# Performance work log

Measured on AMD Instinct MI355X. Metric: run time of the kernel, lower is better.

## Reference

```python
import jax, jax.numpy as jnp
import numpy as np

N, HIDDEN, LATENT, RANK = 131072, 512, 128, 4


def setup_inputs() -> dict:
    key = jax.random.key(0)
    ks = jax.random.split(key, 7)
    s = 1.0 / np.sqrt(HIDDEN)  # fan-in scaling keeps exp(fc_d(x)) well-behaved
    return {
        "x": jax.random.normal(ks[0], (N, HIDDEN), dtype=jnp.float32),
        "W_mu": jax.random.normal(ks[1], (HIDDEN, LATENT), dtype=jnp.float32) * s,
        "b_mu": jnp.zeros((LATENT,), dtype=jnp.float32),
        "W_u": jax.random.normal(ks[2], (HIDDEN, LATENT * RANK), dtype=jnp.float32) * s,
        "b_u": jnp.zeros((LATENT * RANK,), dtype=jnp.float32),
        "W_d": jax.random.normal(ks[3], (HIDDEN, LATENT), dtype=jnp.float32) * s,
        "b_d": jnp.zeros((LATENT,), dtype=jnp.float32),
        "rank": RANK,
    }


def reference(x, W_mu, b_mu, W_u, b_u, W_d, b_d, rank):
    n, _ = x.shape
    latent_dim = W_mu.shape[1]
    # forward(): three dense projections
    mu = x @ W_mu + b_mu                                  # [N, L]
    u = (x @ W_u + b_u).reshape(n, latent_dim, rank)      # [N, L, R]
    d = jnp.exp(x @ W_d + b_d)                            # [N, L]
    # kl_divergence(): batched closed-form KL vs N(0, I), Sigma = diag(d) + U U^T
    trace_Sigma = d.sum(-1) + (u * u).sum((-2, -1))       # [N]
    mu_sq = (mu * mu).sum(-1)                             # [N]
    logdet_diag = jnp.log(d).sum(-1)                      # [N]
    M = u / jnp.sqrt(d)[..., None]                        # [N, L, R]
    MtM = jnp.einsum("nlr,nls->nrs", M, M)                # [N, R, R]
    eigvals = jnp.linalg.eigvalsh(MtM)                    # [N, R]
    logdet_Sigma = logdet_diag + jnp.log1p(eigvals).sum(-1)
    kl = 0.5 * (trace_Sigma + mu_sq - latent_dim - logdet_Sigma)
    return kl.mean()
```

## Files before the change

kernel.cpp:

```cpp
#include <hip/hip_runtime.h>
#include <stdint.h>

typedef __attribute__((ext_vector_type(8))) short bf16x8;
typedef __attribute__((ext_vector_type(4))) float f32x4;

#define NROWS 131072
#define HID   512
#define LAT   128
#define NCOL  768
#define BM    64

static __device__ __forceinline__ short f2bf(float f) {
    union { float f; uint32_t u; } v; v.f = f;
    uint32_t r = v.u + 0x7FFFu + ((v.u >> 16) & 1u);
    return (short)(r >> 16);
}

__global__ void prep_kernel(const float* __restrict__ Wmu, const float* __restrict__ bmu,
                            const float* __restrict__ Wu,  const float* __restrict__ bu,
                            const float* __restrict__ Wd,  const float* __restrict__ bd,
                            short* __restrict__ Bfrag, float* __restrict__ bias,
                            float* __restrict__ out) {
    int t = blockIdx.x * blockDim.x + threadIdx.x;
    const int NFRAG = 48 * 16 * 64;
    if (t < NFRAG) {
        int l  = t & 63;
        int ks = (t >> 6) & 15;
        int n  = t >> 10;
        int col = n * 16 + (l & 15);
        int k0  = ks * 32 + (l >> 4) * 8;
        const float* src; int sc, ld;
        if (col < LAT)          { src = Wmu; sc = col;           ld = LAT;     }
        else if (col < LAT * 5) { src = Wu;  sc = col - LAT;     ld = LAT * 4; }
        else                    { src = Wd;  sc = col - LAT * 5; ld = LAT;     }
        bf16x8 v;
        #pragma unroll
        for (int j = 0; j < 8; ++j) v[j] = f2bf(src[(size_t)(k0 + j) * ld + sc]);
        ((bf16x8*)Bfrag)[t] = v;
    } else if (t < NFRAG + NCOL) {
        int col = t - NFRAG;
        float b;
        if (col < LAT)          b = bmu[col];
        else if (col < LAT * 5) b = bu[col - LAT];
        else                    b = bd[col - LAT * 5];
        bias[col] = b;
    } else if (t == NFRAG + NCOL) {
        *out = 0.0f;
    }
}

__launch_bounds__(512, 2)
__global__ void fused_kernel(const float* __restrict__ x, const short* __restrict__ Bfrag,
                             const float* __restrict__ bias, float* __restrict__ out) {
    __shared__ __align__(16) short Abuf[2][4096];
    __shared__ __align__(16) float Epi[32 * 772];
    __shared__ float bsum;

    const int tid  = threadIdx.x;
    const int l    = tid & 63;
    const int w    = tid >> 6;
    const int row0 = blockIdx.x * BM;

    const int srt  = w & 3;
    const int sks  = w >> 2;
    const int srow = srt * 16 + (l & 15);
    const int skk  = sks * 32 + (l >> 4) * 8;
    const int awr  = ((sks * 4 + srt) * 64 + l) * 8;

    const float*  xrow = x + (size_t)(row0 + srow) * HID + skk;
    const bf16x8* bwp  = (const bf16x8*)Bfrag + (size_t)w * 6 * 16 * 64 + l;

    f32x4 acc[4][6];
    #pragma unroll
    for (int rt = 0; rt < 4; ++rt)
        #pragma unroll
        for (int i = 0; i < 6; ++i) acc[rt][i] = (f32x4){0.f, 0.f, 0.f, 0.f};

    bf16x8 b0[6], b1[6];
    #pragma unroll
    for (int i = 0; i < 6; ++i) b0[i] = bwp[(size_t)i * 16 * 64];

    {
        f32x4 q0 = *(const f32x4*)(xrow);
        f32x4 q1 = *(const f32x4*)(xrow + 4);
        bf16x8 av;
        av[0]=f2bf(q0[0]); av[1]=f2bf(q0[1]); av[2]=f2bf(q0[2]); av[3]=f2bf(q0[3]);
        av[4]=f2bf(q1[0]); av[5]=f2bf(q1[1]); av[6]=f2bf(q1[2]); av[7]=f2bf(q1[3]);
        *(bf16x8*)&Abuf[0][awr] = av;
    }
    if (tid == 0) bsum = 0.0f;
    __syncthreads();

    f32x4 p0, p1;
    #pragma unroll
    for (int c = 0; c < 8; ++c) {
        const int buf = c & 1;
        #pragma unroll
        for (int i = 0; i < 6; ++i) b1[i] = bwp[((size_t)i * 16 + (2 * c + 1)) * 64];
        if (c < 7) {
            const float* xq = xrow + (c + 1) * 64;
            p0 = *(const f32x4*)(xq);
            p1 = *(const f32x4*)(xq + 4);
        }
        #pragma unroll
        for (int rt = 0; rt < 4; ++rt) {
            bf16x8 av = *(const bf16x8*)&Abuf[buf][(rt * 64 + l) * 8];
            #pragma unroll
            for (int i = 0; i < 6; ++i)
                acc[rt][i] = __builtin_amdgcn_mfma_f32_16x16x32_bf16(av, b0[i], acc[rt][i], 0, 0, 0);
        }
        if (c < 7) {
            #pragma unroll
            for (int i = 0; i < 6; ++i) b0[i] = bwp[((size_t)i * 16 + (2 * c + 2)) * 64];
        }
        #pragma unroll
        for (int rt = 0; rt < 4; ++rt) {
            bf16x8 av = *(const bf16x8*)&Abuf[buf][((4 + rt) * 64 + l) * 8];
            #pragma unroll
            for (int i = 0; i < 6; ++i)
                acc[rt][i] = __builtin_amdgcn_mfma_f32_16x16x32_bf16(av, b1[i], acc[rt][i], 0, 0, 0);
        }
        if (c < 7) {
            bf16x8 av;
            av[0]=f2bf(p0[0]); av[1]=f2bf(p0[1]); av[2]=f2bf(p0[2]); av[3]=f2bf(p0[3]);
            av[4]=f2bf(p1[0]); av[5]=f2bf(p1[1]); av[6]=f2bf(p1[2]); av[7]=f2bf(p1[3]);
            *(bf16x8*)&Abuf[buf ^ 1][awr] = av;
            __syncthreads();
        }
    }

    float pre_bias[6];
    #pragma unroll
    for (int i = 0; i < 6; ++i) pre_bias[i] = bias[(w * 6 + i) * 16 + (l & 15)];

    float my_kl = 0.0f;
    const int r16 = tid >> 4;
    const int jj  = tid & 15;

    #pragma unroll
    for (int pass = 0; pass < 2; ++pass) {
        #pragma unroll
        for (int rt2 = 0; rt2 < 2; ++rt2) {
            const int rt    = pass * 2 + rt2;
            const int rbase = rt2 * 16 + (l >> 4) * 4;
            #pragma unroll
            for (int i = 0; i < 6; ++i) {
                const int col = (w * 6 + i) * 16 + (l & 15);
                #pragma unroll
                for (int j = 0; j < 4; ++j)
                    Epi[(rbase + j) * 772 + col] = acc[rt][i][j] + pre_bias[i];
            }
        }
        __syncthreads();

        const float* rowp = &Epi[r16 * 772];
        float s_mu2=0.f, s_u2=0.f, s_d=0.f, s_td=0.f;
        float m00=0.f,m01=0.f,m02=0.f,m03=0.f,m11=0.f,m12=0.f,m13=0.f,m22=0.f,m23=0.f,m33=0.f;
        #pragma unroll
        for (int t8 = 0; t8 < 8; ++t8) {
            const int a = jj + 16 * t8;
            float mu = rowp[a];
            float td = rowp[640 + a];
            f32x4 u4 = *(const f32x4*)&rowp[128 + 4 * a];
            s_mu2 += mu * mu;
            s_td  += td;
            float ed  = __expf(td);
            float eid = __expf(-td);
            s_d  += ed;
            s_u2 += u4[0]*u4[0] + u4[1]*u4[1] + u4[2]*u4[2] + u4[3]*u4[3];
            m00 += u4[0]*u4[0]*eid; m01 += u4[0]*u4[1]*eid;
            m02 += u4[0]*u4[2]*eid; m03 += u4[0]*u4[3]*eid;
            m11 += u4[1]*u4[1]*eid; m12 += u4[1]*u4[2]*eid;
            m13 += u4[1]*u4[3]*eid; m22 += u4[2]*u4[2]*eid;
            m23 += u4[2]*u4[3]*eid; m33 += u4[3]*u4[3]*eid;
        }
        #define XRED(v) { v += __shfl_xor(v,1); v += __shfl_xor(v,2); v += __shfl_xor(v,4); v += __shfl_xor(v,8); }
        XRED(s_mu2) XRED(s_u2) XRED(s_d) XRED(s_td)
        XRED(m00) XRED(m01) XRED(m02) XRED(m03) XRED(m11)
        XRED(m12) XRED(m13) XRED(m22) XRED(m23) XRED(m33)

        if (jj == 0) {
            float a00=1.f+m00, a01=m01, a02=m02, a03=m03;
            float a11=1.f+m11, a12=m12, a13=m13;
            float a22=1.f+m22, a23=m23, a33=1.f+m33;
            float i00 = 1.f / a00;
            float t01=a01*i00, t02=a02*i00, t03=a03*i00;
            a11 -= t01*a01; a12 -= t01*a02; a13 -= t01*a03;
            a22 -= t02*a02; a23 -= t02*a03;
            a33 -= t03*a03;
            float i11 = 1.f / a11;
            float t12=a12*i11, t13=a13*i11;
            a22 -= t12*a12; a23 -= t12*a13;
            a33 -= t13*a13;
            float t23 = a23 / a22;
            a33 -= t23*a23;
            float logdet = __logf(a00 * a11 * a22 * a33);
            my_kl += s_d + s_u2 + s_mu2 - (float)LAT - s_td - logdet;
        }
        __syncthreads();
    }

    my_kl += __shfl_xor(my_kl, 16);
    my_kl += __shfl_xor(my_kl, 32);
    if (l == 0) atomicAdd(&bsum, my_kl);
    __syncthreads();
    if (tid == 0) atomicAdd(out, bsum * (0.5f / (float)NROWS));
}

extern "C" void kernel_launch(void* const* d_in, const int* in_sizes, int n_in,
                              void* d_out, int out_size, void* d_ws, size_t ws_size,
                              hipStream_t stream) {
    (void)in_sizes; (void)n_in; (void)out_size;
    const float* x   = (const float*)d_in[0];
    const float* Wmu = (const float*)d_in[1];
    const float* bmu = (const float*)d_in[2];
    const float* Wu  = (const float*)d_in[3];
    const float* bu  = (const float*)d_in[4];
    const float* Wd  = (const float*)d_in[5];
    const float* bd  = (const float*)d_in[6];
    if (ws_size < (size_t)(48 * 16 * 64 * 16 + NCOL * 4)) return;

    short* Bfrag = (short*)d_ws;
    float* bias  = (float*)((char*)d_ws + 48 * 16 * 64 * 16);
    float* out   = (float*)d_out;

    prep_kernel<<<196, 256, 0, stream>>>(Wmu, bmu, Wu, bu, Wd, bd, Bfrag, bias, out);
    fused_kernel<<<NROWS / BM, 512, 0, stream>>>(x, Bfrag, bias, out);
}
```

Before: 484.6 us.

## Shrink LDS via union, raise occupancy target, deepen x prefetch to two stages

Places the A staging buffer and a smaller 16-row epilogue buffer in one shared-memory union, which cuts LDS per block. That lets the launch bound ask for 4 blocks per CU instead of 2. The epilogue now runs four 16-row passes with 32 threads per row, adding a shuffle step. The x global loads are prefetched two chunks ahead to hide more latency. The higher occupancy target caps registers per thread, so the 96-float accumulator plus prefetch registers may spill.

Result: slower. 1.367 ms (+182.0%).

```diff
diff --git a/kernel.cpp b/kernel.cpp
--- a/kernel.cpp
+++ b/kernel.cpp
@@ -49,11 +49,13 @@
     }
 }
 
-__launch_bounds__(512, 2)
+__launch_bounds__(512, 4)
 __global__ void fused_kernel(const float* __restrict__ x, const short* __restrict__ Bfrag,
                              const float* __restrict__ bias, float* __restrict__ out) {
-    __shared__ __align__(16) short Abuf[2][4096];
-    __shared__ __align__(16) float Epi[32 * 772];
+    __shared__ __align__(16) union {
+        short Abuf[2][4096];
+        float Epi[16 * 772];
+    } S;
     __shared__ float bsum;
 
     const int tid  = threadIdx.x;
@@ -86,25 +88,27 @@
         bf16x8 av;
         av[0]=f2bf(q0[0]); av[1]=f2bf(q0[1]); av[2]=f2bf(q0[2]); av[3]=f2bf(q0[3]);
         av[4]=f2bf(q1[0]); av[5]=f2bf(q1[1]); av[6]=f2bf(q1[2]); av[7]=f2bf(q1[3]);
-        *(bf16x8*)&Abuf[0][awr] = av;
-    }
+        *(bf16x8*)&S.Abuf[0][awr] = av;
+    }
+    f32x4 px[2][2];
+    px[1][0] = *(const f32x4*)(xrow + 64);
+    px[1][1] = *(const f32x4*)(xrow + 64 + 4);
     if (tid == 0) bsum = 0.0f;
     __syncthreads();
 
-    f32x4 p0, p1;
     #pragma unroll
     for (int c = 0; c < 8; ++c) {
         const int buf = c & 1;
         #pragma unroll
         for (int i = 0; i < 6; ++i) b1[i] = bwp[((size_t)i * 16 + (2 * c + 1)) * 64];
-        if (c < 7) {
-            const float* xq = xrow + (c + 1) * 64;
-            p0 = *(const f32x4*)(xq);
-            p1 = *(const f32x4*)(xq + 4);
+        if (c <= 5) {
+            const float* xq = xrow + (c + 2) * 64;
+            px[c & 1][0] = *(const f32x4*)(xq);
+            px[c & 1][1] = *(const f32x4*)(xq + 4);
         }
         #pragma unroll
         for (int rt = 0; rt < 4; ++rt) {
-            bf16x8 av = *(const bf16x8*)&Abuf[buf][(rt * 64 + l) * 8];
+            bf16x8 av = *(const bf16x8*)&S.Abuf[buf][(rt * 64 + l) * 8];
             #pragma unroll
             for (int i = 0; i < 6; ++i)
                 acc[rt][i] = __builtin_amdgcn_mfma_f32_16x16x32_bf16(av, b0[i], acc[rt][i], 0, 0, 0);
@@ -115,16 +119,18 @@
         }
         #pragma unroll
         for (int rt = 0; rt < 4; ++rt) {
-            bf16x8 av = *(const bf16x8*)&Abuf[buf][((4 + rt) * 64 + l) * 8];
+            bf16x8 av = *(const bf16x8*)&S.Abuf[buf][((4 + rt) * 64 + l) * 8];
             #pragma unroll
             for (int i = 0; i < 6; ++i)
                 acc[rt][i] = __builtin_amdgcn_mfma_f32_16x16x32_bf16(av, b1[i], acc[rt][i], 0, 0, 0);
         }
         if (c < 7) {
+            const f32x4 q0 = px[(c + 1) & 1][0];
+            const f32x4 q1 = px[(c + 1) & 1][1];
             bf16x8 av;
-            av[0]=f2bf(p0[0]); av[1]=f2bf(p0[1]); av[2]=f2bf(p0[2]); av[3]=f2bf(p0[3]);
-            av[4]=f2bf(p1[0]); av[5]=f2bf(p1[1]); av[6]=f2bf(p1[2]); av[7]=f2bf(p1[3]);
-            *(bf16x8*)&Abuf[buf ^ 1][awr] = av;
+            av[0]=f2bf(q0[0]); av[1]=f2bf(q0[1]); av[2]=f2bf(q0[2]); av[3]=f2bf(q0[3]);
+            av[4]=f2bf(q1[0]); av[5]=f2bf(q1[1]); av[6]=f2bf(q1[2]); av[7]=f2bf(q1[3]);
+            *(bf16x8*)&S.Abuf[buf ^ 1][awr] = av;
             __syncthreads();
         }
     }
@@ -134,31 +140,30 @@
     for (int i = 0; i < 6; ++i) pre_bias[i] = bias[(w * 6 + i) * 16 + (l & 15)];
 
     float my_kl = 0.0f;
-    const int r16 = tid >> 4;
-    const int jj  = tid & 15;
-
-    #pragma unroll
-    for (int pass = 0; pass < 2; ++pass) {
-        #pragma unroll
-        for (int rt2 = 0; rt2 < 2; ++rt2) {
-            const int rt    = pass * 2 + rt2;
-            const int rbase = rt2 * 16 + (l >> 4) * 4;
+    const int r16 = tid >> 5;
+    const int jj  = tid & 31;
+
+    #pragma unroll
+    for (int pass = 0; pass < 4; ++pass) {
+        __syncthreads();
+        {
+            const int rbase = (l >> 4) * 4;
             #pragma unroll
             for (int i = 0; i < 6; ++i) {
                 const int col = (w * 6 + i) * 16 + (l & 15);
                 #pragma unroll
                 for (int j = 0; j < 4; ++j)
-                    Epi[(rbase + j) * 772 + col] = acc[rt][i][j] + pre_bias[i];
+                    S.Epi[(rbase + j) * 772 + col] = acc[pass][i][j] + pre_bias[i];
             }
         }
         __syncthreads();
 
-        const float* rowp = &Epi[r16 * 772];
+        const float* rowp = &S.Epi[r16 * 772];
         float s_mu2=0.f, s_u2=0.f, s_d=0.f, s_td=0.f;
         float m00=0.f,m01=0.f,m02=0.f,m03=0.f,m11=0.f,m12=0.f,m13=0.f,m22=0.f,m23=0.f,m33=0.f;
         #pragma unroll
-        for (int t8 = 0; t8 < 8; ++t8) {
-            const int a = jj + 16 * t8;
+        for (int t4 = 0; t4 < 4; ++t4) {
+            const int a = jj + 32 * t4;
             float mu = rowp[a];
             float td = rowp[640 + a];
             f32x4 u4 = *(const f32x4*)&rowp[128 + 4 * a];
@@ -174,7 +179,8 @@
             m13 += u4[1]*u4[3]*eid; m22 += u4[2]*u4[2]*eid;
             m23 += u4[2]*u4[3]*eid; m33 += u4[3]*u4[3]*eid;
         }
-        #define XRED(v) { v += __shfl_xor(v,1); v += __shfl_xor(v,2); v += __shfl_xor(v,4); v += __shfl_xor(v,8); }
+        #define XRED(v) { v += __shfl_xor(v,1); v += __shfl_xor(v,2); v += __shfl_xor(v,4); \
+                          v += __shfl_xor(v,8); v += __shfl_xor(v,16); }
         XRED(s_mu2) XRED(s_u2) XRED(s_d) XRED(s_td)
         XRED(m00) XRED(m01) XRED(m02) XRED(m03) XRED(m11)
         XRED(m12) XRED(m13) XRED(m22) XRED(m23) XRED(m33)
@@ -197,10 +203,8 @@
             float logdet = __logf(a00 * a11 * a22 * a33);
             my_kl += s_d + s_u2 + s_mu2 - (float)LAT - s_td - logdet;
         }
-        __syncthreads();
-    }
-
-    my_kl += __shfl_xor(my_kl, 16);
+    }
+
     my_kl += __shfl_xor(my_kl, 32);
     if (l == 0) atomicAdd(&bsum, my_kl);
     __syncthreads();
```
